# Performance work log

Measured on AMD Instinct MI355X. Metric: run time of the kernel, lower is better.

The kernel has to match this reference:

```python
import jax, jax.numpy as jnp
import numpy as np
import math

B, L, CS, CZ = 1, 512, 256, 128
H, CH, PQ, PV = 8, 32, 4, 8
NUM_BLOCKS = 8
CAT = H * CH + H * PV * 3 + H * PV + H * CZ  # 1536


def _ln(x, g, b, eps=1e-5):
    mu = jnp.mean(x, -1, keepdims=True)
    var = jnp.mean((x - mu) ** 2, -1, keepdims=True)
    return (x - mu) * jax.lax.rsqrt(var + eps) * g + b


def _quat_to_rot(bq, cq, dq):
    # BackboneUpdate: quaternion with implicit a=1, normalized (AF2 Alg. 23)
    norm = jnp.sqrt(1.0 + bq * bq + cq * cq + dq * dq)
    a = 1.0 / norm
    b = bq / norm
    c = cq / norm
    d = dq / norm
    return jnp.stack([
        jnp.stack([a * a + b * b - c * c - d * d, 2 * (b * c - a * d), 2 * (b * d + a * c)], -1),
        jnp.stack([2 * (b * c + a * d), a * a - b * b + c * c - d * d, 2 * (c * d - a * b)], -1),
        jnp.stack([2 * (b * d - a * c), 2 * (c * d + a * b), a * a - b * b - c * c + d * d], -1),
    ], -2)


def _forward(s, z, mask, ln_s_g, ln_s_b, ln_z_g, ln_z_b, w_init, b_init,
             ln_ipa_g, ln_ipa_b, ln_tr_g, ln_tr_b,
             wq, bq, wk, bk, wv, bv, wqp, bqp, wkp, bkp, wvp, bvp,
             wpb, head_w, wo, bo, wt1, bt1, wt2, bt2, wt3, bt3, wbb, bbb):
    s0 = _ln(s, ln_s_g, ln_s_b)
    zn = _ln(z, ln_z_g, ln_z_b)
    sc = s0 @ w_init + b_init
    R = jnp.broadcast_to(jnp.eye(3, dtype=s.dtype), (B, L, 3, 3))
    t = jnp.zeros((B, L, 3), s.dtype)
    wL = math.sqrt(1.0 / 3.0)
    wC = math.sqrt(2.0 / (9.0 * PQ))
    gamma = jax.nn.softplus(head_w)  # [H]
    pair_bias = jnp.einsum('bijc,ch->bhij', zn, wpb)
    mask_bias = (mask[:, None, None, :] - 1.0) * 1e9
    for i in range(NUM_BLOCKS):
        # ---- Invariant Point Attention (AF2 Alg. 22, shared weights) ----
        q = (sc @ wq + bq).reshape(B, L, H, CH)
        k = (sc @ wk + bk).reshape(B, L, H, CH)
        v = (sc @ wv + bv).reshape(B, L, H, CH)
        qp = (sc @ wqp + bqp).reshape(B, L, H, PQ, 3)
        kp = (sc @ wkp + bkp).reshape(B, L, H, PQ, 3)
        vp = (sc @ wvp + bvp).reshape(B, L, H, PV, 3)
        tb = t[:, :, None, None, :]
        qpg = jnp.einsum('blij,blhpj->blhpi', R, qp) + tb  # local -> global
        kpg = jnp.einsum('blij,blhpj->blhpi', R, kp) + tb
        vpg = jnp.einsum('blij,blhpj->blhpi', R, vp) + tb
        scal = jnp.einsum('bihc,bjhc->bhij', q, k) / math.sqrt(CH)
        # sum_p ||qpg_i - kpg_j||^2 via |q|^2 + |k|^2 - 2 q.k (avoids [B,L,L,H,P,3])
        qk = jnp.einsum('bihpx,bjhpx->bhij', qpg, kpg)
        qn = jnp.moveaxis(jnp.sum(qpg ** 2, axis=(-2, -1)), -1, 1)  # [B,H,L]
        kn = jnp.moveaxis(jnp.sum(kpg ** 2, axis=(-2, -1)), -1, 1)
        d2 = qn[..., :, None] + kn[..., None, :] - 2.0 * qk  # [B,H,L,L]
        logits = wL * (scal + pair_bias - 0.5 * wC * gamma[None, :, None, None] * d2) + mask_bias
        a = jax.nn.softmax(logits, axis=-1)
        o = jnp.einsum('bhij,bjhc->bihc', a, v).reshape(B, L, H * CH)
        optg = jnp.einsum('bhij,bjhpx->bihpx', a, vpg)
        optl = jnp.einsum('blji,blhpj->blhpi', R, optg - tb)  # R^T (o - t)
        onrm = jnp.sqrt(jnp.sum(optl ** 2, -1) + 1e-8)  # [B,L,H,PV]
        opair = jnp.einsum('bhij,bijc->bihc', a, zn).reshape(B, L, H * CZ)
        cat = jnp.concatenate([o, optl.reshape(B, L, H * PV * 3), onrm.reshape(B, L, H * PV), opair], -1)
        ipa_up = cat @ wo + bo
        sc = _ln(sc + ipa_up, ln_ipa_g, ln_ipa_b)  # dropout = identity (eval)
        # ---- transition ----
        tr = jax.nn.relu(sc @ wt1 + bt1)
        tr = jax.nn.relu(tr @ wt2 + bt2)
        tr = (tr @ wt3 + bt3) * mask[..., None]
        sc = _ln(sc + tr, ln_tr_g, ln_tr_b)
        # ---- backbone update + frame composition ----
        upd = sc @ wbb + bbb  # [B,L,6]
        dR = _quat_to_rot(upd[..., 0], upd[..., 1], upd[..., 2])
        dt = upd[..., 3:6] * mask[..., None]
        t = jnp.einsum('blij,blj->bli', R, dt) + t
        R = jnp.einsum('blij,bljk->blik', R, dR)
        if i < NUM_BLOCKS - 1:
            R = jax.lax.stop_gradient(R)  # stop_rotation_gradients
    return sc, R, t


def setup_inputs() -> dict:
    key = jax.random.key(0)
    ks = jax.random.split(key, 20)
    w = lambda k, shape, sc=0.05: jax.random.normal(k, shape, jnp.float32) * sc
    inp = dict(
        s=jax.random.normal(ks[0], (B, L, CS), jnp.float32),
        z=jax.random.normal(ks[1], (B, L, L, CZ), jnp.float32),
        mask=jnp.ones((B, L), jnp.float32),
        ln_s_g=jnp.ones((CS,), jnp.float32), ln_s_b=jnp.zeros((CS,), jnp.float32),
        ln_z_g=jnp.ones((CZ,), jnp.float32), ln_z_b=jnp.zeros((CZ,), jnp.float32),
        w_init=w(ks[2], (CS, CS)), b_init=jnp.zeros((CS,), jnp.float32),
        ln_ipa_g=jnp.ones((CS,), jnp.float32), ln_ipa_b=jnp.zeros((CS,), jnp.float32),
        ln_tr_g=jnp.ones((CS,), jnp.float32), ln_tr_b=jnp.zeros((CS,), jnp.float32),
        wq=w(ks[3], (CS, H * CH)), bq=jnp.zeros((H * CH,), jnp.float32),
        wk=w(ks[4], (CS, H * CH)), bk=jnp.zeros((H * CH,), jnp.float32),
        wv=w(ks[5], (CS, H * CH)), bv=jnp.zeros((H * CH,), jnp.float32),
        wqp=w(ks[6], (CS, H * PQ * 3)), bqp=jnp.zeros((H * PQ * 3,), jnp.float32),
        wkp=w(ks[7], (CS, H * PQ * 3)), bkp=jnp.zeros((H * PQ * 3,), jnp.float32),
        wvp=w(ks[8], (CS, H * PV * 3)), bvp=jnp.zeros((H * PV * 3,), jnp.float32),
        wpb=w(ks[9], (CZ, H)),
        head_w=jnp.zeros((H,), jnp.float32),
        wo=w(ks[10], (CAT, CS), 0.02), bo=jnp.zeros((CS,), jnp.float32),
        wt1=w(ks[11], (CS, CS)), bt1=jnp.zeros((CS,), jnp.float32),
        wt2=w(ks[12], (CS, CS)), bt2=jnp.zeros((CS,), jnp.float32),
        wt3=w(ks[13], (CS, CS)), bt3=jnp.zeros((CS,), jnp.float32),
        wbb=w(ks[14], (CS, 6)), bbb=jnp.zeros((6,), jnp.float32),
    )
    return inp


def reference(s, z, mask, ln_s_g, ln_s_b, ln_z_g, ln_z_b, w_init, b_init,
              ln_ipa_g, ln_ipa_b, ln_tr_g, ln_tr_b,
              wq, bq, wk, bk, wv, bv, wqp, bqp, wkp, bkp, wvp, bvp,
              wpb, head_w, wo, bo, wt1, bt1, wt2, bt2, wt3, bt3, wbb, bbb):
    return _forward(s, z, mask, ln_s_g, ln_s_b, ln_z_g, ln_z_b, w_init, b_init,
                    ln_ipa_g, ln_ipa_b, ln_tr_g, ln_tr_b,
                    wq, bq, wk, bk, wv, bv, wqp, bqp, wkp, bkp, wvp, bvp,
                    wpb, head_w, wo, bo, wt1, bt1, wt2, bt2, wt3, bt3, wbb, bbb)
```

## Files before the change

### kernel.cpp

```cpp
#include <hip/hip_runtime.h>
#include <hip/hip_bf16.h>
#include <hip/hip_fp16.h>
#include <math.h>

#define Lq 512
#define CSd 256
#define CZd 128
#define Hd 8
#define CHd 32
#define PQd 4
#define PVd 8
#define CATd 1536
#define NPROJ 1152

typedef __attribute__((ext_vector_type(4))) float floatx4;
typedef __attribute__((ext_vector_type(8))) short shortx8;

#define OFF_SC      0
#define OFF_PB      393216
#define OFF_P       1441792
#define OFF_QN      2031616
#define OFF_KN      2035712
#define OFF_A16     2039808
#define OFF_CAT     4136960
#define OFF_S0      4923392
#define OFF_R       5054464
#define OFF_T       5059072
#define OFF_GAMMA   5060608
#define OFF_MASKB   5060616
#define OFF_BCAT    5061128
#define OFF_WINITP  5062280
#define OFF_WT1P    5127816
#define OFF_WT2P    5193352
#define OFF_WT3P    5258888
#define OFF_WOP     5324424
#define OFF_WCATP   5717640
#define OFF_QP      6012552
#define OFF_KP      6274696
#define OFF_VP      6536840
#define OFF_ZNT     6798984

#define WLC 0.57735026918962576f
#define WCC 0.23570226039551584f
#define ISC 0.17677669529663687f

__device__ __forceinline__ float wave_sum(float v){
  #pragma unroll
  for (int m=32; m; m>>=1) v += __shfl_xor(v, m);
  return v;
}
__device__ __forceinline__ short f2bf(float v){
  __hip_bfloat16 h = (__hip_bfloat16)v;
  return __builtin_bit_cast(short, h);
}
__device__ __forceinline__ float bf2f(short s){
  unsigned u = ((unsigned)(unsigned short)s) << 16;
  return __builtin_bit_cast(float, u);
}
__device__ __forceinline__ __hip_bfloat16 s2b(short s){
  return __builtin_bit_cast(__hip_bfloat16, s);
}

__global__ __launch_bounds__(256) void k_setup(
    const float* __restrict__ bq, const float* __restrict__ bk, const float* __restrict__ bv,
    const float* __restrict__ bqp, const float* __restrict__ bkp, const float* __restrict__ bvp,
    const float* __restrict__ head_w, const float* __restrict__ mask,
    float* __restrict__ bcat, float* __restrict__ gamma,
    float* __restrict__ maskb, float* __restrict__ R, float* __restrict__ t){
  int k = blockIdx.x*256 + threadIdx.x;
  if (k < NPROJ){
    float v;
    if      (k < 256) v = bq[k];
    else if (k < 512) v = bk[k-256];
    else if (k < 768) v = bv[k-512];
    else if (k < 864) v = bqp[k-768];
    else if (k < 960) v = bkp[k-864];
    else              v = bvp[k-960];
    bcat[k] = v;
    return;
  }
  k -= NPROJ;
  if (k < Hd){ gamma[k] = log1pf(expf(head_w[k])); return; }
  k -= Hd;
  if (k < Lq){ maskb[k] = (mask[k] - 1.f)*1e9f; return; }
  k -= Lq;
  if (k < Lq){
    #pragma unroll
    for (int ii=0; ii<9; ii++) R[k*9+ii] = (ii==0||ii==4||ii==8) ? 1.f : 0.f;
    t[k*3] = 0.f; t[k*3+1] = 0.f; t[k*3+2] = 0.f;
  }
}

__global__ __launch_bounds__(256) void k_pack(
    const float* __restrict__ W, int K, int N, __hip_bfloat16* __restrict__ out){
  int idx = blockIdx.x*256 + threadIdx.x;
  if (idx >= K*N) return;
  int j = idx & 7, lane = (idx>>3) & 63, rest = idx >> 9;
  int nt = N >> 4;
  int tn = rest % nt, tk = rest / nt;
  int k = tk*32 + (lane>>4)*8 + j;
  int n = tn*16 + (lane&15);
  float v = W[(size_t)k*N + n];
  short h = f2bf(v);
  short l = f2bf(v - bf2f(h));
  size_t base = (size_t)rest*1024 + (idx & 511);
  out[base]       = s2b(h);
  out[base + 512] = s2b(l);
}

__global__ __launch_bounds__(256) void k_pack_cat(
    const float* __restrict__ wq, const float* __restrict__ wk, const float* __restrict__ wv,
    const float* __restrict__ wqp, const float* __restrict__ wkp, const float* __restrict__ wvp,
    __hip_bfloat16* __restrict__ out){
  int idx = blockIdx.x*256 + threadIdx.x;
  if (idx >= CSd*NPROJ) return;
  int j = idx & 7, lane = (idx>>3) & 63, rest = idx >> 9;
  const int nt = NPROJ >> 4;
  int tn = rest % nt, tk = rest / nt;
  int k = tk*32 + (lane>>4)*8 + j;
  int n = tn*16 + (lane&15);
  float v;
  if      (n < 256) v = wq[k*256 + n];
  else if (n < 512) v = wk[k*256 + n-256];
  else if (n < 768) v = wv[k*256 + n-512];
  else if (n < 864) v = wqp[k*96 + n-768];
  else if (n < 960) v = wkp[k*96 + n-864];
  else              v = wvp[k*192 + n-960];
  short h = f2bf(v);
  short l = f2bf(v - bf2f(h));
  size_t base = (size_t)rest*1024 + (idx & 511);
  out[base]       = s2b(h);
  out[base + 512] = s2b(l);
}

template<int NST>
__global__ __launch_bounds__(256) void k_gemm_mfma(
    const float* __restrict__ A, int K,
    const __hip_bfloat16* __restrict__ Bp, int N,
    const float* __restrict__ bias,
    float* __restrict__ Cf,
    int relu, const float* __restrict__ rowscale){
  int tid = threadIdx.x;
  int wave = tid>>6, lane = tid&63;
  int i0 = blockIdx.y*64 + wave*16;
  int n0 = blockIdx.x*(NST*16);
  int quad = lane>>4, l16 = lane&15;
  floatx4 acc[NST] = {};
  const int ntiles = N >> 4;
  const float* arow = A + (size_t)(i0 + l16)*K + quad*8;
  const __hip_bfloat16* bbase = Bp + ((size_t)(n0>>4))*1024 + (size_t)(lane&63)*8;
  for (int k0=0; k0<K; k0+=32){
    float4 v0 = *(const float4*)(arow + k0);
    float4 v1 = *(const float4*)(arow + k0 + 4);
    float av[8] = {v0.x,v0.y,v0.z,v0.w,v1.x,v1.y,v1.z,v1.w};
    shortx8 ahi, alo;
    #pragma unroll
    for (int j=0; j<8; j++){
      short h = f2bf(av[j]);
      ahi[j] = h;
      alo[j] = f2bf(av[j] - bf2f(h));
    }
    const __hip_bfloat16* bt = bbase + (size_t)(k0>>5)*ntiles*1024;
    #pragma unroll
    for (int s=0; s<NST; s++){
      shortx8 bhi = *(const shortx8*)(bt + s*1024);
      shortx8 blo = *(const shortx8*)(bt + s*1024 + 512);
      acc[s] = __builtin_amdgcn_mfma_f32_16x16x32_bf16(ahi, bhi, acc[s], 0, 0, 0);
      acc[s] = __builtin_amdgcn_mfma_f32_16x16x32_bf16(alo, bhi, acc[s], 0, 0, 0);
      acc[s] = __builtin_amdgcn_mfma_f32_16x16x32_bf16(ahi, blo, acc[s], 0, 0, 0);
    }
  }
  #pragma unroll
  for (int s=0; s<NST; s++){
    int n = n0 + s*16 + l16;
    float bs = bias ? bias[n] : 0.f;
    #pragma unroll
    for (int r=0; r<4; r++){
      int m = i0 + quad*4 + r;
      float v = acc[s][r] + bs;
      if (relu) v = fmaxf(v, 0.f);
      if (rowscale) v *= rowscale[m];
      Cf[(size_t)m*N + n] = v;
    }
  }
}

__global__ __launch_bounds__(256) void k_gemm_ipa(
    const float* __restrict__ A, const __hip_bfloat16* __restrict__ Bp,
    const float* __restrict__ bias, float* __restrict__ C0, float* __restrict__ C1){
  int tid = threadIdx.x;
  int wave = tid>>6, lane = tid&63;
  int ks = blockIdx.y >> 3;
  int i0 = (blockIdx.y & 7)*64 + wave*16;
  int n0 = blockIdx.x*16;
  int quad = lane>>4, l16 = lane&15;
  floatx4 acc = {};
  const float* arow = A + (size_t)(i0 + l16)*CATd + ks*768 + quad*8;
  const __hip_bfloat16* bbase = Bp + ((size_t)(ks*24*16 + (n0>>4)))*1024 + (size_t)lane*8;
  for (int k0=0; k0<768; k0+=32){
    float4 v0 = *(const float4*)(arow + k0);
    float4 v1 = *(const float4*)(arow + k0 + 4);
    float av[8] = {v0.x,v0.y,v0.z,v0.w,v1.x,v1.y,v1.z,v1.w};
    shortx8 ahi, alo;
    #pragma unroll
    for (int j=0; j<8; j++){
      short h = f2bf(av[j]);
      ahi[j] = h;
      alo[j] = f2bf(av[j] - bf2f(h));
    }
    const __hip_bfloat16* bt = bbase + (size_t)(k0>>5)*16*1024;
    shortx8 bhi = *(const shortx8*)bt;
    shortx8 blo = *(const shortx8*)(bt + 512);
    acc = __builtin_amdgcn_mfma_f32_16x16x32_bf16(ahi, bhi, acc, 0, 0, 0);
    acc = __builtin_amdgcn_mfma_f32_16x16x32_bf16(alo, bhi, acc, 0, 0, 0);
    acc = __builtin_amdgcn_mfma_f32_16x16x32_bf16(ahi, blo, acc, 0, 0, 0);
  }
  float* C = ks ? C1 : C0;
  int n = n0 + l16;
  float bs = ks ? 0.f : bias[n];
  #pragma unroll
  for (int r=0; r<4; r++)
    C[(size_t)(i0 + quad*4 + r)*CSd + n] = acc[r] + bs;
}

__global__ __launch_bounds__(256) void k_addln(
    const float* __restrict__ x, const float* __restrict__ y,
    const float* __restrict__ g, const float* __restrict__ b,
    float* __restrict__ out){
  __shared__ float red[4];
  int row = blockIdx.x, tid = threadIdx.x;
  float v = x[row*CSd + tid];
  if (y) v += y[row*CSd + tid];
  int wid = tid>>6, lane = tid&63;
  float s = wave_sum(v);
  if (lane==0) red[wid] = s;
  __syncthreads();
  float mu = (red[0]+red[1]+red[2]+red[3]) * (1.f/CSd);
  __syncthreads();
  float d = v - mu;
  float s2 = wave_sum(d*d);
  if (lane==0) red[wid] = s2;
  __syncthreads();
  float var = (red[0]+red[1]+red[2]+red[3]) * (1.f/CSd);
  float rs = rsqrtf(var + 1e-5f);
  out[row*CSd + tid] = d*rs*g[tid] + b[tid];
}

__global__ __launch_bounds__(1024, 4) void k_lnz_pb(
    const float* __restrict__ z, const float* __restrict__ g, const float* __restrict__ b,
    const float* __restrict__ wpb, __half* __restrict__ pb, __hip_bfloat16* __restrict__ znt){
  __shared__ float Zt[64*129];
  __shared__ float wpbl[128*12];
  __shared__ float gl[128], bl[128];
  int tid = threadIdx.x;
  size_t row0 = (size_t)blockIdx.x*64;
  int ib = (int)(row0 >> 9), j0 = (int)(row0 & 511);
  {
    int c = tid>>3, h = tid&7;
    wpbl[c*12 + h] = wpb[tid];
  }
  if (tid < 128){ gl[tid] = g[tid]; bl[tid] = b[tid]; }
  {
    int w = tid>>6, lane = tid&63;
    #pragma unroll
    for (int it=0; it<4; it++){
      int row = it*16 + w;
      const float2 v = *(const float2*)(z + (row0+row)*(size_t)CZd + lane*2);
      Zt[row*129 + lane*2]     = v.x;
      Zt[row*129 + lane*2 + 1] = v.y;
    }
  }
  __syncthreads();
  {
    int r = tid>>4, q = tid&15;
    int rot = 2*(q>>2);
    float S1=0.f, S2=0.f;
    float zv[8];
    #pragma unroll
    for (int i=0; i<8; i++){
      int ii = (i + rot) & 7;
      float v = Zt[r*129 + q*8 + ii];
      zv[i] = v;
      S1 += v; S2 += v*v;
    }
    S1 += __shfl_xor(S1,1); S2 += __shfl_xor(S2,1);
    S1 += __shfl_xor(S1,2); S2 += __shfl_xor(S2,2);
    S1 += __shfl_xor(S1,4); S2 += __shfl_xor(S2,4);
    S1 += __shfl_xor(S1,8); S2 += __shfl_xor(S2,8);
    float mu = S1 * (1.f/128.f);
    float var = S2 * (1.f/128.f) - mu*mu;
    float rs = rsqrtf(var + 1e-5f);
    float d[8] = {};
    #pragma unroll
    for (int i=0; i<8; i++){
      int ii = (i + rot) & 7;
      int c = q*8 + ii;
      float znv = (zv[i]-mu)*rs*gl[c] + bl[c];
      Zt[r*129 + c] = znv;
      const float4 w0 = *(const float4*)&wpbl[c*12];
      const float4 w1 = *(const float4*)&wpbl[c*12 + 4];
      d[0] += znv*w0.x; d[1] += znv*w0.y; d[2] += znv*w0.z; d[3] += znv*w0.w;
      d[4] += znv*w1.x; d[5] += znv*w1.y; d[6] += znv*w1.z; d[7] += znv*w1.w;
    }
    #pragma unroll
    for (int h=0; h<8; h++){
      d[h] += __shfl_xor(d[h],1);
      d[h] += __shfl_xor(d[h],2);
      d[h] += __shfl_xor(d[h],4);
      d[h] += __shfl_xor(d[h],8);
    }
    if (q == 0){
      #pragma unroll
      for (int h=0; h<8; h++)
        pb[((size_t)(h*Lq + ib))*Lq + j0 + r] = __float2half(d[h]);
    }
  }
  __syncthreads();
  {
    int jj = (tid&31)*2, cidx = tid>>5;
    unsigned short* zo = (unsigned short*)znt;
    #pragma unroll
    for (int it=0; it<4; it++){
      int c = it*32 + cidx;
      float z0 = Zt[jj*129 + c];
      float z1 = Zt[(jj+1)*129 + c];
      unsigned int o = ((unsigned int)(unsigned short)f2bf(z0)) |
                       (((unsigned int)(unsigned short)f2bf(z1)) << 16);
      *(unsigned int*)(zo + ((size_t)(ib*128 + c))*512 + j0 + jj) = o;
    }
  }
}

__global__ __launch_bounds__(256) void k_packqkv(
    const float* __restrict__ P, const float* __restrict__ R, const float* __restrict__ t,
    const float* __restrict__ gamma, int zfill,
    float* __restrict__ Qp, __hip_bfloat16* __restrict__ Kp, __hip_bfloat16* __restrict__ Vp,
    float* __restrict__ qn, float* __restrict__ kn){
  int idx = blockIdx.x*256 + threadIdx.x;
  int region = idx >> 15;
  int rem = idx & 32767;
  if (region == 0){
    int oct = rem & 7, h = (rem>>3)&7, j = rem>>6;
    float v[8] = {0.f,0.f,0.f,0.f,0.f,0.f,0.f,0.f};
    const float* Prow = P + (size_t)j*NPROJ;
    if (oct < 4){
      float4 a = *(const float4*)(Prow + 256 + h*CHd + oct*8);
      float4 b4 = *(const float4*)(Prow + 256 + h*CHd + oct*8 + 4);
      v[0]=a.x; v[1]=a.y; v[2]=a.z; v[3]=a.w; v[4]=b4.x; v[5]=b4.y; v[6]=b4.z; v[7]=b4.w;
    } else if (oct < 6){
      const float* kp = Prow + 864 + h*12;
      float4 k0 = *(const float4*)kp;
      float4 k1 = *(const float4*)(kp+4);
      float4 k2 = *(const float4*)(kp+8);
      float kv[12] = {k0.x,k0.y,k0.z,k0.w,k1.x,k1.y,k1.z,k1.w,k2.x,k2.y,k2.z,k2.w};
      float Rl[9];
      #pragma unroll
      for (int ii=0; ii<9; ii++) Rl[ii] = R[j*9+ii];
      float tv[3] = {t[j*3], t[j*3+1], t[j*3+2]};
      float gvals[12];
      #pragma unroll
      for (int p=0; p<4; p++)
        #pragma unroll
        for (int ax=0; ax<3; ax++)
          gvals[p*3+ax] = Rl[ax*3]*kv[p*3] + Rl[ax*3+1]*kv[p*3+1] + Rl[ax*3+2]*kv[p*3+2] + tv[ax];
      if (oct == 4){
        #pragma unroll
        for (int m=0; m<8; m++) v[m] = gvals[m];
      } else {
        #pragma unroll
        for (int m=0; m<4; m++) v[m] = gvals[8+m];
        float acc = 0.f;
        #pragma unroll
        for (int m=0; m<12; m++) acc += gvals[m]*gvals[m];
        kn[j*Hd + h] = acc;
      }
    } else {
      if (!zfill) return;
    }
    shortx8 hi, lo;
    #pragma unroll
    for (int m=0; m<8; m++){
      short hh = f2bf(v[m]);
      hi[m] = hh; lo[m] = f2bf(v[m] - bf2f(hh));
    }
    int kc = oct>>2, jt = j>>4, l16 = j&15, quad = oct&3;
    size_t base = (size_t)((h*2+kc)*32 + jt)*1024 + (quad*16+l16)*8;
    short* kp16 = (short*)Kp;
    *(shortx8*)(kp16 + base)       = hi;
    *(shortx8*)(kp16 + base + 512) = lo;
  } else if (region == 1){
    int n = rem & 63, h = (rem>>6)&7, jg = rem>>9;
    int jb = jg*8;
    float v[8] = {0.f,0.f,0.f,0.f,0.f,0.f,0.f,0.f};
    if (n < 32){
      #pragma unroll
      for (int m=0; m<8; m++) v[m] = P[(size_t)(jb+m)*NPROJ + 512 + h*CHd + n];
    } else if (n < 56){
      int p = (n-32)/3, ax = (n-32)%3;
      #pragma unroll
      for (int m=0; m<8; m++){
        int j = jb+m;
        const float* vp = P + (size_t)j*NPROJ + 960 + h*24 + p*3;
        const float* Rr = R + j*9 + ax*3;
        v[m] = Rr[0]*vp[0] + Rr[1]*vp[1] + Rr[2]*vp[2] + t[j*3+ax];
      }
    } else {
      if (!zfill) return;
    }
    shortx8 hi, lo;
    #pragma unroll
    for (int m=0; m<8; m++){
      short hh = f2bf(v[m]);
      hi[m] = hh; lo[m] = f2bf(v[m] - bf2f(hh));
    }
    int kc2 = jg>>2, w = n>>4, l16 = n&15, quad = jg&3;
    size_t base = (size_t)((h*16+kc2)*4 + w)*1024 + (quad*16+l16)*8;
    short* vp16 = (short*)Vp;
    *(shortx8*)(vp16 + base)       = hi;
    *(shortx8*)(vp16 + base + 512) = lo;
  } else {
    int oct = rem & 7, h = (rem>>3)&7, i = rem>>6;
    float v[8] = {0.f,0.f,0.f,0.f,0.f,0.f,0.f,0.f};
    const float* Prow = P + (size_t)i*NPROJ;
    if (oct < 4){
      float4 a = *(const float4*)(Prow + h*CHd + oct*8);
      float4 b4 = *(const float4*)(Prow + h*CHd + oct*8 + 4);
      const float sc = WLC*ISC;
      v[0]=a.x*sc; v[1]=a.y*sc; v[2]=a.z*sc; v[3]=a.w*sc;
      v[4]=b4.x*sc; v[5]=b4.y*sc; v[6]=b4.z*sc; v[7]=b4.w*sc;
    } else if (oct < 6){
      const float* qp = Prow + 768 + h*12;
      float4 k0 = *(const float4*)qp;
      float4 k1 = *(const float4*)(qp+4);
      float4 k2 = *(const float4*)(qp+8);
      float kv[12] = {k0.x,k0.y,k0.z,k0.w,k1.x,k1.y,k1.z,k1.w,k2.x,k2.y,k2.z,k2.w};
      float Rl[9];
      #pragma unroll
      for (int ii=0; ii<9; ii++) Rl[ii] = R[i*9+ii];
      float tv[3] = {t[i*3], t[i*3+1], t[i*3+2]};
      float gvals[12];
      #pragma unroll
      for (int p=0; p<4; p++)
        #pragma unroll
        for (int ax=0; ax<3; ax++)
          gvals[p*3+ax] = Rl[ax*3]*kv[p*3] + Rl[ax*3+1]*kv[p*3+1] + Rl[ax*3+2]*kv[p*3+2] + tv[ax];
      float sc = WLC*WCC*gamma[h];
      if (oct == 4){
        #pragma unroll
        for (int m=0; m<8; m++) v[m] = gvals[m]*sc;
      } else {
        #pragma unroll
        for (int m=0; m<4; m++) v[m] = gvals[8+m]*sc;
        float acc = 0.f;
        #pragma unroll
        for (int m=0; m<12; m++) acc += gvals[m]*gvals[m];
        qn[i*Hd + h] = acc;
      }
    } else {
      if (!zfill) return;
    }
    float* qrow = Qp + ((size_t)h*512 + i)*64 + oct*8;
    *(float4*)qrow       = make_float4(v[0],v[1],v[2],v[3]);
    *(float4*)(qrow + 4) = make_float4(v[4],v[5],v[6],v[7]);
  }
}

__global__ __launch_bounds__(512) void k_attn(
    const float* __restrict__ Qp, const __hip_bfloat16* __restrict__ Kp,
    const __hip_bfloat16* __restrict__ Vp,
    const float* __restrict__ qn, const float* __restrict__ kn,
    const __half* __restrict__ pb, const float* __restrict__ maskb,
    const float* __restrict__ gamma,
    const float* __restrict__ R, const float* __restrict__ t,
    __hip_bfloat16* __restrict__ a16hi,
    float* __restrict__ cat){
  __shared__ float At[8][516];
  __shared__ short AbfH[16*4*16*8];
  __shared__ short AbfL[16*4*16*8];
  __shared__ float Ot[8][36];
  __shared__ float Pv[8][68];
  __shared__ float qnL[8];
  int tid = threadIdx.x;
  int i0 = blockIdx.x*8, h = blockIdx.y;
  int wave = tid>>6, lane = tid&63, quad = lane>>4, l16 = lane&15;
  int half = wave>>2, w4 = wave&3;
  float gam = gamma[h];
  float coef = 0.5f*WLC*WCC*gam;
  if (tid < 8) qnL[tid] = qn[(i0+tid)*Hd + h];
  __syncthreads();
  const float* qrow = Qp + ((size_t)h*512 + i0 + (l16&7))*64 + quad*8;
  shortx8 qhi[2], qlo[2];
  #pragma unroll
  for (int kc=0; kc<2; kc++){
    float4 v0 = *(const float4*)(qrow + kc*32);
    float4 v1 = *(const float4*)(qrow + kc*32 + 4);
    float av[8] = {v0.x,v0.y,v0.z,v0.w,v1.x,v1.y,v1.z,v1.w};
    #pragma unroll
    for (int j=0; j<8; j++){
      short hh = f2bf(av[j]);
      qhi[kc][j] = hh; qlo[kc][j] = f2bf(av[j] - bf2f(hh));
    }
  }
  #pragma unroll
  for (int it=0; it<4; it++){
    int jt = it*8 + wave;
    floatx4 acc = {};
    #pragma unroll
    for (int kc=0; kc<2; kc++){
      const __hip_bfloat16* bt = Kp + (size_t)((h*2+kc)*32 + jt)*1024 + lane*8;
      shortx8 bhi = *(const shortx8*)bt;
      shortx8 blo = *(const shortx8*)(bt + 512);
      acc = __builtin_amdgcn_mfma_f32_16x16x32_bf16(qhi[kc], bhi, acc, 0, 0, 0);
      acc = __builtin_amdgcn_mfma_f32_16x16x32_bf16(qlo[kc], bhi, acc, 0, 0, 0);
      acc = __builtin_amdgcn_mfma_f32_16x16x32_bf16(qhi[kc], blo, acc, 0, 0, 0);
    }
    if (quad < 2){
      int j = jt*16 + l16;
      float knj = kn[j*Hd + h];
      float mbj = maskb[j];
      #pragma unroll
      for (int r=0; r<4; r++){
        int i = quad*4 + r;
        float pbv = __half2float(pb[((size_t)(h*Lq) + i0 + i)*Lq + j]);
        At[i][j] = acc[r] + WLC*pbv + mbj - coef*(qnL[i] + knj);
      }
    }
  }
  __syncthreads();
  {
    int w = wave;
    float v[8];
    float m = -1e30f;
    #pragma unroll
    for (int k=0; k<8; k++){ v[k] = At[w][lane + 64*k]; m = fmaxf(m, v[k]); }
    #pragma unroll
    for (int msk=32; msk; msk>>=1) m = fmaxf(m, __shfl_xor(m, msk));
    float ssum = 0.f;
    #pragma unroll
    for (int k=0; k<8; k++){ float e = __expf(v[k]-m); v[k]=e; ssum += e; }
    #pragma unroll
    for (int msk=32; msk; msk>>=1) ssum += __shfl_xor(ssum, msk);
    float inv = 1.f/ssum;
    #pragma unroll
    for (int k=0; k<8; k++){
      int cc = lane + 64*k;
      float p = v[k]*inv;
      short hh = f2bf(p);
      short ll = f2bf(p - bf2f(hh));
      a16hi[(((size_t)(i0+w)*16 + (cc>>5))*8 + h)*32 + (cc&31)] = s2b(hh);
      int base = ((cc>>5)*4 + ((cc>>3)&3))*16;
      int off0 = ((base + w)<<3) + (cc&7);
      int off1 = ((base + w + 8)<<3) + (cc&7);
      AbfH[off0] = hh; AbfH[off1] = hh;
      AbfL[off0] = ll; AbfL[off1] = ll;
    }
  }
  __syncthreads();
  floatx4 acc2 = {};
  #pragma unroll
  for (int kk=0; kk<8; kk++){
    int kc2 = half*8 + kk;
    int aoff = (((kc2*4 + quad)*16 + l16))<<3;
    shortx8 ahi = *(const shortx8*)&AbfH[aoff];
    shortx8 alo = *(const shortx8*)&AbfL[aoff];
    const __hip_bfloat16* bt = Vp + (size_t)((h*16+kc2)*4 + w4)*1024 + lane*8;
    shortx8 bhi = *(const shortx8*)bt;
    shortx8 blo = *(const shortx8*)(bt + 512);
    acc2 = __builtin_amdgcn_mfma_f32_16x16x32_bf16(ahi, bhi, acc2, 0, 0, 0);
    acc2 = __builtin_amdgcn_mfma_f32_16x16x32_bf16(alo, bhi, acc2, 0, 0, 0);
    acc2 = __builtin_amdgcn_mfma_f32_16x16x32_bf16(ahi, blo, acc2, 0, 0, 0);
  }
  if (half == 1 && quad < 2){
    #pragma unroll
    for (int r=0;r<4;r++) Pv[quad*4+r][w4*16+l16] = acc2[r];
  }
  __syncthreads();
  if (half == 0 && quad < 2){
    int n = w4*16 + l16;
    #pragma unroll
    for (int r=0;r<4;r++){
      int i = quad*4+r;
      float v = acc2[r] + Pv[i][n];
      if (n < 32) cat[(size_t)(i0+i)*CATd + h*CHd + n] = v;
      else        Ot[i][n-32] = v;
    }
  }
  __syncthreads();
  if (tid < 64){
    int i = tid>>3, p = tid&7, gi = i0+i;
    float o0 = Ot[i][p*3], o1 = Ot[i][p*3+1], o2 = Ot[i][p*3+2];
    float d0 = o0 - t[gi*3], d1 = o1 - t[gi*3+1], d2 = o2 - t[gi*3+2];
    const float* Rm = R + gi*9;
    float l0 = Rm[0]*d0 + Rm[3]*d1 + Rm[6]*d2;
    float l1 = Rm[1]*d0 + Rm[4]*d1 + Rm[7]*d2;
    float l2 = Rm[2]*d0 + Rm[5]*d1 + Rm[8]*d2;
    float* cr = cat + (size_t)gi*CATd;
    cr[256 + h*24 + p*3]   = l0;
    cr[256 + h*24 + p*3+1] = l1;
    cr[256 + h*24 + p*3+2] = l2;
    cr[448 + h*8 + p] = sqrtf(l0*l0 + l1*l1 + l2*l2 + 1e-8f);
  }
}

__global__ __launch_bounds__(512) void k_opair_mfma(
    const __hip_bfloat16* __restrict__ a16hi,
    const __hip_bfloat16* __restrict__ znt, float* __restrict__ cat){
  int i = blockIdx.x;
  int tid = threadIdx.x;
  int wave = tid>>6, lane = tid&63, quad = lane>>4, l16 = lane&15;
  int nt = wave;
  floatx4 acc = {};
  const __hip_bfloat16* abase_h = a16hi + ((size_t)i*16*8 + (l16&7))*32 + quad*8;
  const __hip_bfloat16* zb = znt + ((size_t)i*128 + nt*16 + l16)*512 + quad*8;
  #pragma unroll
  for (int kt=0; kt<16; kt++){
    shortx8 ah = *(const shortx8*)(abase_h + kt*256);
    shortx8 b0 = *(const shortx8*)(zb + kt*32);
    acc = __builtin_amdgcn_mfma_f32_16x16x32_bf16(ah, b0, acc, 0, 0, 0);
  }
  if (quad < 2){
    float* cr = cat + (size_t)i*CATd + 512;
    #pragma unroll
    for (int r=0; r<4; r++){
      int h = quad*4 + r;
      cr[h*CZd + nt*16 + l16] = acc[r];
    }
  }
}

__device__ __forceinline__ void gemm_bf8(
    const short* __restrict__ AHp, const short* __restrict__ ALp,
    short* __restrict__ OH, short* __restrict__ OL, float (*Yf)[260],
    const __hip_bfloat16* __restrict__ Wp, const float* __restrict__ bias,
    bool relu, int tid){
  int wave = tid>>6, lane = tid&63, quad = lane>>4, l16 = lane&15;
  floatx4 acc[2] = {};
  for (int kc=0; kc<8; kc++){
    int aoff = (((kc*4 + quad)*16 + l16))<<3;
    shortx8 ahi = *(const shortx8*)&AHp[aoff];
    shortx8 alo = *(const shortx8*)&ALp[aoff];
    #pragma unroll
    for (int ns=0; ns<2; ns++){
      const __hip_bfloat16* bt = Wp + (size_t)(kc*16 + wave*2 + ns)*1024 + lane*8;
      shortx8 bhi = *(const shortx8*)bt;
      shortx8 blo = *(const shortx8*)(bt + 512);
      acc[ns] = __builtin_amdgcn_mfma_f32_16x16x32_bf16(ahi, bhi, acc[ns], 0, 0, 0);
      acc[ns] = __builtin_amdgcn_mfma_f32_16x16x32_bf16(alo, bhi, acc[ns], 0, 0, 0);
      acc[ns] = __builtin_amdgcn_mfma_f32_16x16x32_bf16(ahi, blo, acc[ns], 0, 0, 0);
    }
  }
  #pragma unroll
  for (int ns=0; ns<2; ns++){
    int n = (wave*2+ns)*16 + l16;
    float bs = bias[n];
    #pragma unroll
    for (int r=0;r<4;r++){
      float v = acc[ns][r] + bs;
      if (relu) v = fmaxf(v, 0.f);
      int row = quad*4 + r;
      if (OH){
        short hh = f2bf(v);
        int off = ((((n>>5)*4 + ((n>>3)&3))*16 + row)<<3) + (n&7);
        OH[off] = hh;
        OL[off] = f2bf(v - bf2f(hh));
      } else {
        Yf[row][n] = v;
      }
    }
  }
}

__global__ __launch_bounds__(512) void k_mega(
    float* __restrict__ scb, const float* __restrict__ ipa, const float* __restrict__ ipa2,
    const float* __restrict__ gi_, const float* __restrict__ bi_,
    const __hip_bfloat16* __restrict__ W1, const float* __restrict__ c1,
    const __hip_bfloat16* __restrict__ W2, const float* __restrict__ c2,
    const __hip_bfloat16* __restrict__ W3, const float* __restrict__ c3,
    const float* __restrict__ gt_, const float* __restrict__ bt_,
    const float* __restrict__ mask,
    const float* __restrict__ wbb, const float* __restrict__ bbb,
    float* __restrict__ R, float* __restrict__ t){
  __shared__ float As[16][260], Bs[16][260];
  __shared__ short AH[2][4096], AL[2][4096];
  __shared__ float rA[16][33], rB[16][33];
  __shared__ float mv[16][2];
  __shared__ float u6p[16][6][2];
  int tid = threadIdx.x;
  int i0 = blockIdx.x*16;
  int r = tid>>5, c5 = tid&31, c0 = c5*8;
  float v[8];
  {
    const float* sr = scb + (size_t)(i0+r)*CSd + c0;
    const float* ir = ipa + (size_t)(i0+r)*CSd + c0;
    const float* ir2 = ipa2 + (size_t)(i0+r)*CSd + c0;
    float s1=0.f, s2=0.f;
    #pragma unroll
    for (int k2=0;k2<8;k2++){ float x = sr[k2] + ir[k2] + ir2[k2]; v[k2]=x; s1+=x; s2+=x*x; }
    rA[r][c5]=s1; rB[r][c5]=s2;
  }
  __syncthreads();
  if (tid<16){
    float s1=0.f,s2=0.f;
    #pragma unroll
    for (int c=0;c<32;c++){ s1+=rA[tid][c]; s2+=rB[tid][c]; }
    float mu = s1*(1.f/CSd), var = s2*(1.f/CSd) - mu*mu;
    mv[tid][0]=mu; mv[tid][1]=rsqrtf(var+1e-5f);
  }
  __syncthreads();
  {
    float mu=mv[r][0], rs=mv[r][1];
    #pragma unroll
    for (int k2=0;k2<8;k2++){
      int col = c0+k2;
      float o = (v[k2]-mu)*rs*gi_[col] + bi_[col];
      As[r][col] = o;
      short hh = f2bf(o);
      int off = ((((col>>5)*4 + ((col>>3)&3))*16 + r)<<3) + (col&7);
      AH[0][off] = hh;
      AL[0][off] = f2bf(o - bf2f(hh));
    }
  }
  __syncthreads();
  gemm_bf8(AH[0], AL[0], AH[1], AL[1], nullptr, W1, c1, true, tid);
  __syncthreads();
  gemm_bf8(AH[1], AL[1], AH[0], AL[0], nullptr, W2, c2, true, tid);
  __syncthreads();
  gemm_bf8(AH[0], AL[0], nullptr, nullptr, Bs, W3, c3, false, tid);
  __syncthreads();
  {
    float mk = mask[i0+r];
    float s1=0.f, s2=0.f;
    #pragma unroll
    for (int k2=0;k2<8;k2++){ float x = As[r][c0+k2] + Bs[r][c0+k2]*mk; v[k2]=x; s1+=x; s2+=x*x; }
    rA[r][c5]=s1; rB[r][c5]=s2;
  }
  __syncthreads();
  if (tid<16){
    float s1=0.f,s2=0.f;
    #pragma unroll
    for (int c=0;c<32;c++){ s1+=rA[tid][c]; s2+=rB[tid][c]; }
    float mu = s1*(1.f/CSd), var = s2*(1.f/CSd) - mu*mu;
    mv[tid][0]=mu; mv[tid][1]=rsqrtf(var+1e-5f);
  }
  __syncthreads();
  {
    float mu=mv[r][0], rs=mv[r][1];
    float* out = scb + (size_t)(i0+r)*CSd + c0;
    #pragma unroll
    for (int k2=0;k2<8;k2++){
      int col = c0+k2;
      float o = (v[k2]-mu)*rs*gt_[col] + bt_[col];
      As[r][col] = o;
      out[k2] = o;
    }
  }
  __syncthreads();
  if (tid < 192){
    int rr = tid/12, o = (tid%12)>>1, half = tid&1;
    float acc = half ? 0.f : bbb[o];
    int kb = half*128;
    for (int k2=kb; k2<kb+128; k2++) acc += As[rr][k2]*wbb[k2*6+o];
    u6p[rr][o][half] = acc;
  }
  __syncthreads();
  if (tid < 16){
    int gidx = i0 + tid;
    float uu[6];
    #pragma unroll
    for (int o=0;o<6;o++) uu[o] = u6p[tid][o][0] + u6p[tid][o][1];
    float bq = uu[0], cq = uu[1], dq = uu[2];
    float norm = sqrtf(1.f + bq*bq + cq*cq + dq*dq);
    float a = 1.f/norm, b_ = bq/norm, c_ = cq/norm, d_ = dq/norm;
    float dR[9];
    dR[0] = a*a + b_*b_ - c_*c_ - d_*d_; dR[1] = 2.f*(b_*c_ - a*d_); dR[2] = 2.f*(b_*d_ + a*c_);
    dR[3] = 2.f*(b_*c_ + a*d_); dR[4] = a*a - b_*b_ + c_*c_ - d_*d_; dR[5] = 2.f*(c_*d_ - a*b_);
    dR[6] = 2.f*(b_*d_ - a*c_); dR[7] = 2.f*(c_*d_ + a*b_); dR[8] = a*a - b_*b_ - c_*c_ + d_*d_;
    float mk = mask[gidx];
    float dt0 = uu[3]*mk, dt1 = uu[4]*mk, dt2 = uu[5]*mk;
    float Rm[9];
    #pragma unroll
    for (int ii=0; ii<9; ii++) Rm[ii] = R[gidx*9+ii];
    t[gidx*3]   += Rm[0]*dt0 + Rm[1]*dt1 + Rm[2]*dt2;
    t[gidx*3+1] += Rm[3]*dt0 + Rm[4]*dt1 + Rm[5]*dt2;
    t[gidx*3+2] += Rm[6]*dt0 + Rm[7]*dt1 + Rm[8]*dt2;
    #pragma unroll
    for (int ii=0; ii<3; ii++)
      #pragma unroll
      for (int jj=0; jj<3; jj++)
        R[gidx*9 + ii*3 + jj] = Rm[ii*3]*dR[jj] + Rm[ii*3+1]*dR[3+jj] + Rm[ii*3+2]*dR[6+jj];
  }
}

__global__ __launch_bounds__(256) void k_writeout(
    const float* __restrict__ sc, const float* __restrict__ R, const float* __restrict__ t,
    float* __restrict__ out){
  int idx = blockIdx.x*256 + threadIdx.x;
  if      (idx < 131072) out[idx] = sc[idx];
  else if (idx < 135680) out[idx] = R[idx-131072];
  else if (idx < 137216) out[idx] = t[idx-135680];
}

extern "C" void kernel_launch(void* const* d_in, const int* in_sizes, int n_in,
                              void* d_out, int out_size, void* d_ws, size_t ws_size,
                              hipStream_t stream){
  const float* s      = (const float*)d_in[0];
  const float* z      = (const float*)d_in[1];
  const float* mask   = (const float*)d_in[2];
  const float* ln_s_g = (const float*)d_in[3];
  const float* ln_s_b = (const float*)d_in[4];
  const float* ln_z_g = (const float*)d_in[5];
  const float* ln_z_b = (const float*)d_in[6];
  const float* w_init = (const float*)d_in[7];
  const float* b_init = (const float*)d_in[8];
  const float* ln_ipa_g = (const float*)d_in[9];
  const float* ln_ipa_b = (const float*)d_in[10];
  const float* ln_tr_g  = (const float*)d_in[11];
  const float* ln_tr_b  = (const float*)d_in[12];
  const float* wq = (const float*)d_in[13]; const float* bq = (const float*)d_in[14];
  const float* wk = (const float*)d_in[15]; const float* bk = (const float*)d_in[16];
  const float* wv = (const float*)d_in[17]; const float* bv = (const float*)d_in[18];
  const float* wqp = (const float*)d_in[19]; const float* bqp = (const float*)d_in[20];
  const float* wkp = (const float*)d_in[21]; const float* bkp = (const float*)d_in[22];
  const float* wvp = (const float*)d_in[23]; const float* bvp = (const float*)d_in[24];
  const float* wpb = (const float*)d_in[25];
  const float* head_w = (const float*)d_in[26];
  const float* wo = (const float*)d_in[27]; const float* bo = (const float*)d_in[28];
  const float* wt1 = (const float*)d_in[29]; const float* bt1 = (const float*)d_in[30];
  const float* wt2 = (const float*)d_in[31]; const float* bt2 = (const float*)d_in[32];
  const float* wt3 = (const float*)d_in[33]; const float* bt3 = (const float*)d_in[34];
  const float* wbb = (const float*)d_in[35]; const float* bbb = (const float*)d_in[36];

  float* W = (float*)d_ws;
  float* scb   = W + OFF_SC;
  __half*  pbb  = (__half*)(W + OFF_PB);
  float* Pb    = W + OFF_P;
  float* ipa2b = W + OFF_P + 262144;
  float* qnb   = W + OFF_QN;
  float* knb   = W + OFF_KN;
  __hip_bfloat16* a16hi = (__hip_bfloat16*)(W + OFF_A16);
  float* catb  = W + OFF_CAT;
  float* s0b   = W + OFF_S0;
  float* Rb    = W + OFF_R;
  float* tb    = W + OFF_T;
  float* gammab= W + OFF_GAMMA;
  float* maskb = W + OFF_MASKB;
  float* bcat  = W + OFF_BCAT;
  __hip_bfloat16* WinitP = (__hip_bfloat16*)(W + OFF_WINITP);
  __hip_bfloat16* Wt1P   = (__hip_bfloat16*)(W + OFF_WT1P);
  __hip_bfloat16* Wt2P   = (__hip_bfloat16*)(W + OFF_WT2P);
  __hip_bfloat16* Wt3P   = (__hip_bfloat16*)(W + OFF_WT3P);
  __hip_bfloat16* WoP    = (__hip_bfloat16*)(W + OFF_WOP);
  __hip_bfloat16* WcatP  = (__hip_bfloat16*)(W + OFF_WCATP);
  float* Qp = W + OFF_QP;
  __hip_bfloat16* Kp = (__hip_bfloat16*)(W + OFF_KP);
  __hip_bfloat16* Vp = (__hip_bfloat16*)(W + OFF_VP);
  __hip_bfloat16* znt = (__hip_bfloat16*)(W + OFF_ZNT);

  k_setup<<<9, 256, 0, stream>>>(bq,bk,bv,bqp,bkp,bvp, head_w, mask, bcat, gammab, maskb, Rb, tb);
  k_pack_cat<<<CSd*NPROJ/256, 256, 0, stream>>>(wq,wk,wv,wqp,wkp,wvp, WcatP);
  k_pack<<<256,  256, 0, stream>>>(w_init, CSd, CSd, WinitP);
  k_pack<<<1536, 256, 0, stream>>>(wo, CATd, CSd, WoP);
  k_pack<<<256,  256, 0, stream>>>(wt1, CSd, CSd, Wt1P);
  k_pack<<<256,  256, 0, stream>>>(wt2, CSd, CSd, Wt2P);
  k_pack<<<256,  256, 0, stream>>>(wt3, CSd, CSd, Wt3P);

  k_addln<<<Lq, 256, 0, stream>>>(s, nullptr, ln_s_g, ln_s_b, s0b);
  k_gemm_mfma<4><<<dim3(4,8), 256, 0, stream>>>(s0b, CSd, WinitP, CSd, b_init, scb, 0, nullptr);
  k_lnz_pb<<<Lq*Lq/64, 1024, 0, stream>>>(z, ln_z_g, ln_z_b, wpb, pbb, znt);

  for (int it=0; it<8; ++it){
    k_gemm_mfma<2><<<dim3(36,8), 256, 0, stream>>>(scb, CSd, WcatP, NPROJ, bcat, Pb, 0, nullptr);
    k_packqkv<<<384, 256, 0, stream>>>(Pb, Rb, tb, gammab, (it==0)?1:0,
                                       Qp, Kp, Vp, qnb, knb);
    k_attn<<<dim3(64,8), 512, 0, stream>>>(Qp, Kp, Vp, qnb, knb, pbb, maskb, gammab, Rb, tb,
                                           a16hi, catb);
    k_opair_mfma<<<Lq, 512, 0, stream>>>(a16hi, znt, catb);
    k_gemm_ipa<<<dim3(16,16), 256, 0, stream>>>(catb, WoP, bo, Pb, ipa2b);
    k_mega<<<32, 512, 0, stream>>>(scb, Pb, ipa2b, ln_ipa_g, ln_ipa_b,
                                   Wt1P, bt1, Wt2P, bt2, Wt3P, bt3,
                                   ln_tr_g, ln_tr_b, mask, wbb, bbb, Rb, tb);
  }
  k_writeout<<<536, 256, 0, stream>>>(scb, Rb, tb, (float*)d_out);
}
```

Before: 887.6 us.

## Pre-split projection inputs to bf16, widen attention tiles, retune LN-z stores

```diff
diff --git a/kernel.cpp b/kernel.cpp
--- a/kernel.cpp
+++ b/kernel.cpp
@@ -38,7 +38,8 @@
 #define OFF_QP      6012552
 #define OFF_KP      6274696
 #define OFF_VP      6536840
-#define OFF_ZNT     6798984
+#define OFF_SCA16   6798984
+#define OFF_ZNT     6930056
 
 #define WLC 0.57735026918962576f
 #define WCC 0.23570226039551584f
@@ -185,6 +186,62 @@
   }
 }
 
+__global__ __launch_bounds__(256) void k_cvtA(
+    const float* __restrict__ sc, short* __restrict__ scA16){
+  int idx = blockIdx.x*256 + threadIdx.x;
+  int i = idx>>5, c5 = idx&31;
+  int c0 = c5*8, kc = c5>>2, quad = c5&3;
+  float4 v0 = *(const float4*)(sc + (size_t)i*CSd + c0);
+  float4 v1 = *(const float4*)(sc + (size_t)i*CSd + c0 + 4);
+  float av[8] = {v0.x,v0.y,v0.z,v0.w,v1.x,v1.y,v1.z,v1.w};
+  shortx8 hi, lo;
+  #pragma unroll
+  for (int j=0; j<8; j++){
+    short h = f2bf(av[j]);
+    hi[j] = h; lo[j] = f2bf(av[j] - bf2f(h));
+  }
+  size_t off = ((size_t)(kc*512 + i)*4 + quad)*8;
+  *(shortx8*)(scA16 + off)          = hi;
+  *(shortx8*)(scA16 + off + 131072) = lo;
+}
+
+__global__ __launch_bounds__(256) void k_gemm_proj(
+    const short* __restrict__ scA16,
+    const __hip_bfloat16* __restrict__ Bp,
+    const float* __restrict__ bias,
+    float* __restrict__ Cf){
+  int tid = threadIdx.x;
+  int wave = tid>>6, lane = tid&63;
+  int i0 = blockIdx.y*64 + wave*16;
+  int n0 = blockIdx.x*32;
+  int quad = lane>>4, l16 = lane&15;
+  floatx4 acc[2] = {};
+  const short* abase = scA16 + ((size_t)(i0 + l16)*4 + quad)*8;
+  const __hip_bfloat16* bbase = Bp + ((size_t)(n0>>4))*1024 + (size_t)lane*8;
+  #pragma unroll
+  for (int kc=0; kc<8; kc++){
+    shortx8 ahi = *(const shortx8*)(abase + kc*16384);
+    shortx8 alo = *(const shortx8*)(abase + kc*16384 + 131072);
+    const __hip_bfloat16* bt = bbase + (size_t)kc*72*1024;
+    #pragma unroll
+    for (int s=0; s<2; s++){
+      shortx8 bhi = *(const shortx8*)(bt + s*1024);
+      shortx8 blo = *(const shortx8*)(bt + s*1024 + 512);
+      acc[s] = __builtin_amdgcn_mfma_f32_16x16x32_bf16(ahi, bhi, acc[s], 0, 0, 0);
+      acc[s] = __builtin_amdgcn_mfma_f32_16x16x32_bf16(alo, bhi, acc[s], 0, 0, 0);
+      acc[s] = __builtin_amdgcn_mfma_f32_16x16x32_bf16(ahi, blo, acc[s], 0, 0, 0);
+    }
+  }
+  #pragma unroll
+  for (int s=0; s<2; s++){
+    int n = n0 + s*16 + l16;
+    float bs = bias[n];
+    #pragma unroll
+    for (int r=0; r<4; r++)
+      Cf[(size_t)(i0 + quad*4 + r)*NPROJ + n] = acc[s][r] + bs;
+  }
+}
+
 __global__ __launch_bounds__(256) void k_gemm_ipa(
     const float* __restrict__ A, const __hip_bfloat16* __restrict__ Bp,
     const float* __restrict__ bias, float* __restrict__ C0, float* __restrict__ C1){
@@ -250,14 +307,14 @@
     const float* __restrict__ z, const float* __restrict__ g, const float* __restrict__ b,
     const float* __restrict__ wpb, __half* __restrict__ pb, __hip_bfloat16* __restrict__ znt){
   __shared__ float Zt[64*129];
-  __shared__ float wpbl[128*12];
+  __shared__ float wpbht[8*129];
   __shared__ float gl[128], bl[128];
   int tid = threadIdx.x;
   size_t row0 = (size_t)blockIdx.x*64;
   int ib = (int)(row0 >> 9), j0 = (int)(row0 & 511);
   {
     int c = tid>>3, h = tid&7;
-    wpbl[c*12 + h] = wpb[tid];
+    wpbht[h*129 + c] = wpb[tid];
   }
   if (tid < 128){ gl[tid] = g[tid]; bl[tid] = b[tid]; }
   {
@@ -297,10 +354,8 @@
       int c = q*8 + ii;
       float znv = (zv[i]-mu)*rs*gl[c] + bl[c];
       Zt[r*129 + c] = znv;
-      const float4 w0 = *(const float4*)&wpbl[c*12];
-      const float4 w1 = *(const float4*)&wpbl[c*12 + 4];
-      d[0] += znv*w0.x; d[1] += znv*w0.y; d[2] += znv*w0.z; d[3] += znv*w0.w;
-      d[4] += znv*w1.x; d[5] += znv*w1.y; d[6] += znv*w1.z; d[7] += znv*w1.w;
+      #pragma unroll
+      for (int h=0; h<8; h++) d[h] += znv * wpbht[h*129 + c];
     }
     #pragma unroll
     for (int h=0; h<8; h++){
@@ -317,17 +372,19 @@
   }
   __syncthreads();
   {
-    int jj = (tid&31)*2, cidx = tid>>5;
+    int c = tid>>3, jg = tid&7;
+    int jb = jg*8;
+    unsigned int o[4];
+    #pragma unroll
+    for (int k=0; k<4; k++){
+      float z0 = Zt[(jb+2*k)*129 + c];
+      float z1 = Zt[(jb+2*k+1)*129 + c];
+      o[k] = ((unsigned int)(unsigned short)f2bf(z0)) |
+             (((unsigned int)(unsigned short)f2bf(z1)) << 16);
+    }
     unsigned short* zo = (unsigned short*)znt;
-    #pragma unroll
-    for (int it=0; it<4; it++){
-      int c = it*32 + cidx;
-      float z0 = Zt[jj*129 + c];
-      float z1 = Zt[(jj+1)*129 + c];
-      unsigned int o = ((unsigned int)(unsigned short)f2bf(z0)) |
-                       (((unsigned int)(unsigned short)f2bf(z1)) << 16);
-      *(unsigned int*)(zo + ((size_t)(ib*128 + c))*512 + j0 + jj) = o;
-    }
+    uint4 pk = make_uint4(o[0],o[1],o[2],o[3]);
+    *(uint4*)(zo + ((size_t)(ib*128 + c))*512 + j0 + jb) = pk;
   }
 }
 
@@ -465,7 +522,7 @@
   }
 }
 
-__global__ __launch_bounds__(512) void k_attn(
+__global__ __launch_bounds__(1024) void k_attn(
     const float* __restrict__ Qp, const __hip_bfloat16* __restrict__ Kp,
     const __hip_bfloat16* __restrict__ Vp,
     const float* __restrict__ qn, const float* __restrict__ kn,
@@ -474,21 +531,21 @@
     const float* __restrict__ R, const float* __restrict__ t,
     __hip_bfloat16* __restrict__ a16hi,
     float* __restrict__ cat){
-  __shared__ float At[8][516];
+  __shared__ float At[16][516];
   __shared__ short AbfH[16*4*16*8];
   __shared__ short AbfL[16*4*16*8];
-  __shared__ float Ot[8][36];
-  __shared__ float Pv[8][68];
-  __shared__ float qnL[8];
+  __shared__ float Pv[3][16][68];
+  __shared__ float Ot[16][36];
+  __shared__ float qnL[16];
   int tid = threadIdx.x;
-  int i0 = blockIdx.x*8, h = blockIdx.y;
+  int i0 = blockIdx.x*16, h = blockIdx.y;
   int wave = tid>>6, lane = tid&63, quad = lane>>4, l16 = lane&15;
-  int half = wave>>2, w4 = wave&3;
+  int kg = wave>>2, ng = wave&3;
   float gam = gamma[h];
   float coef = 0.5f*WLC*WCC*gam;
-  if (tid < 8) qnL[tid] = qn[(i0+tid)*Hd + h];
-  __syncthreads();
-  const float* qrow = Qp + ((size_t)h*512 + i0 + (l16&7))*64 + quad*8;
+  if (tid < 16) qnL[tid] = qn[(i0+tid)*Hd + h];
+  __syncthreads();
+  const float* qrow = Qp + ((size_t)h*512 + i0 + l16)*64 + quad*8;
   shortx8 qhi[2], qlo[2];
   #pragma unroll
   for (int kc=0; kc<2; kc++){
@@ -502,8 +559,8 @@
     }
   }
   #pragma unroll
-  for (int it=0; it<4; it++){
-    int jt = it*8 + wave;
+  for (int it=0; it<2; it++){
+    int jt = it*16 + wave;
     floatx4 acc = {};
     #pragma unroll
     for (int kc=0; kc<2; kc++){
@@ -514,16 +571,14 @@
       acc = __builtin_amdgcn_mfma_f32_16x16x32_bf16(qlo[kc], bhi, acc, 0, 0, 0);
       acc = __builtin_amdgcn_mfma_f32_16x16x32_bf16(qhi[kc], blo, acc, 0, 0, 0);
     }
-    if (quad < 2){
-      int j = jt*16 + l16;
-      float knj = kn[j*Hd + h];
-      float mbj = maskb[j];
-      #pragma unroll
-      for (int r=0; r<4; r++){
-        int i = quad*4 + r;
-        float pbv = __half2float(pb[((size_t)(h*Lq) + i0 + i)*Lq + j]);
-        At[i][j] = acc[r] + WLC*pbv + mbj - coef*(qnL[i] + knj);
-      }
+    int j = jt*16 + l16;
+    float knj = kn[j*Hd + h];
+    float mbj = maskb[j];
+    #pragma unroll
+    for (int r=0; r<4; r++){
+      int i = quad*4 + r;
+      float pbv = __half2float(pb[((size_t)(h*Lq) + i0 + i)*Lq + j]);
+      At[i][j] = acc[r] + WLC*pbv + mbj - coef*(qnL[i] + knj);
     }
   }
   __syncthreads();
@@ -548,45 +603,43 @@
       short hh = f2bf(p);
       short ll = f2bf(p - bf2f(hh));
       a16hi[(((size_t)(i0+w)*16 + (cc>>5))*8 + h)*32 + (cc&31)] = s2b(hh);
-      int base = ((cc>>5)*4 + ((cc>>3)&3))*16;
-      int off0 = ((base + w)<<3) + (cc&7);
-      int off1 = ((base + w + 8)<<3) + (cc&7);
-      AbfH[off0] = hh; AbfH[off1] = hh;
-      AbfL[off0] = ll; AbfL[off1] = ll;
+      int off = ((((cc>>5)*4 + ((cc>>3)&3))*16 + w)<<3) + (cc&7);
+      AbfH[off] = hh;
+      AbfL[off] = ll;
     }
   }
   __syncthreads();
   floatx4 acc2 = {};
   #pragma unroll
-  for (int kk=0; kk<8; kk++){
-    int kc2 = half*8 + kk;
+  for (int kk=0; kk<4; kk++){
+    int kc2 = kg*4 + kk;
     int aoff = (((kc2*4 + quad)*16 + l16))<<3;
     shortx8 ahi = *(const shortx8*)&AbfH[aoff];
     shortx8 alo = *(const shortx8*)&AbfL[aoff];
-    const __hip_bfloat16* bt = Vp + (size_t)((h*16+kc2)*4 + w4)*1024 + lane*8;
+    const __hip_bfloat16* bt = Vp + (size_t)((h*16+kc2)*4 + ng)*1024 + lane*8;
     shortx8 bhi = *(const shortx8*)bt;
     shortx8 blo = *(const shortx8*)(bt + 512);
     acc2 = __builtin_amdgcn_mfma_f32_16x16x32_bf16(ahi, bhi, acc2, 0, 0, 0);
     acc2 = __builtin_amdgcn_mfma_f32_16x16x32_bf16(alo, bhi, acc2, 0, 0, 0);
     acc2 = __builtin_amdgcn_mfma_f32_16x16x32_bf16(ahi, blo, acc2, 0, 0, 0);
   }
-  if (half == 1 && quad < 2){
-    #pragma unroll
-    for (int r=0;r<4;r++) Pv[quad*4+r][w4*16+l16] = acc2[r];
-  }
-  __syncthreads();
-  if (half == 0 && quad < 2){
-    int n = w4*16 + l16;
+  if (kg > 0){
+    #pragma unroll
+    for (int r=0;r<4;r++) Pv[kg-1][quad*4+r][ng*16+l16] = acc2[r];
+  }
+  __syncthreads();
+  if (kg == 0){
+    int n = ng*16 + l16;
     #pragma unroll
     for (int r=0;r<4;r++){
       int i = quad*4+r;
-      float v = acc2[r] + Pv[i][n];
+      float v = acc2[r] + Pv[0][i][n] + Pv[1][i][n] + Pv[2][i][n];
       if (n < 32) cat[(size_t)(i0+i)*CATd + h*CHd + n] = v;
       else        Ot[i][n-32] = v;
     }
   }
   __syncthreads();
-  if (tid < 64){
+  if (tid < 128){
     int i = tid>>3, p = tid&7, gi = i0+i;
     float o0 = Ot[i][p*3], o1 = Ot[i][p*3+1], o2 = Ot[i][p*3+2];
     float d0 = o0 - t[gi*3], d1 = o1 - t[gi*3+1], d2 = o2 - t[gi*3+2];
@@ -679,7 +732,7 @@
     const float* __restrict__ gt_, const float* __restrict__ bt_,
     const float* __restrict__ mask,
     const float* __restrict__ wbb, const float* __restrict__ bbb,
-    float* __restrict__ R, float* __restrict__ t){
+    float* __restrict__ R, float* __restrict__ t, short* __restrict__ scA16){
   __shared__ float As[16][260], Bs[16][260];
   __shared__ short AH[2][4096], AL[2][4096];
   __shared__ float rA[16][33], rB[16][33];
@@ -746,13 +799,19 @@
   {
     float mu=mv[r][0], rs=mv[r][1];
     float* out = scb + (size_t)(i0+r)*CSd + c0;
+    shortx8 hi, lo;
     #pragma unroll
     for (int k2=0;k2<8;k2++){
       int col = c0+k2;
       float o = (v[k2]-mu)*rs*gt_[col] + bt_[col];
       As[r][col] = o;
       out[k2] = o;
-    }
+      short hh = f2bf(o);
+      hi[k2] = hh; lo[k2] = f2bf(o - bf2f(hh));
+    }
+    size_t off = ((size_t)((c5>>2)*512 + i0 + r)*4 + (c5&3))*8;
+    *(shortx8*)(scA16 + off)          = hi;
+    *(shortx8*)(scA16 + off + 131072) = lo;
   }
   __syncthreads();
   if (tid < 192){
@@ -854,6 +913,7 @@
   float* Qp = W + OFF_QP;
   __hip_bfloat16* Kp = (__hip_bfloat16*)(W + OFF_KP);
   __hip_bfloat16* Vp = (__hip_bfloat16*)(W + OFF_VP);
+  short* scA16 = (short*)(W + OFF_SCA16);
   __hip_bfloat16* znt = (__hip_bfloat16*)(W + OFF_ZNT);
 
   k_setup<<<9, 256, 0, stream>>>(bq,bk,bv,bqp,bkp,bvp, head_w, mask, bcat, gammab, maskb, Rb, tb);
@@ -866,19 +926,20 @@
 
   k_addln<<<Lq, 256, 0, stream>>>(s, nullptr, ln_s_g, ln_s_b, s0b);
   k_gemm_mfma<4><<<dim3(4,8), 256, 0, stream>>>(s0b, CSd, WinitP, CSd, b_init, scb, 0, nullptr);
+  k_cvtA<<<64, 256, 0, stream>>>(scb, scA16);
   k_lnz_pb<<<Lq*Lq/64, 1024, 0, stream>>>(z, ln_z_g, ln_z_b, wpb, pbb, znt);
 
   for (int it=0; it<8; ++it){
-    k_gemm_mfma<2><<<dim3(36,8), 256, 0, stream>>>(scb, CSd, WcatP, NPROJ, bcat, Pb, 0, nullptr);
+    k_gemm_proj<<<dim3(36,8), 256, 0, stream>>>(scA16, WcatP, bcat, Pb);
     k_packqkv<<<384, 256, 0, stream>>>(Pb, Rb, tb, gammab, (it==0)?1:0,
                                        Qp, Kp, Vp, qnb, knb);
-    k_attn<<<dim3(64,8), 512, 0, stream>>>(Qp, Kp, Vp, qnb, knb, pbb, maskb, gammab, Rb, tb,
-                                           a16hi, catb);
+    k_attn<<<dim3(32,8), 1024, 0, stream>>>(Qp, Kp, Vp, qnb, knb, pbb, maskb, gammab, Rb, tb,
+                                            a16hi, catb);
     k_opair_mfma<<<Lq, 512, 0, stream>>>(a16hi, znt, catb);
     k_gemm_ipa<<<dim3(16,16), 256, 0, stream>>>(catb, WoP, bo, Pb, ipa2b);
     k_mega<<<32, 512, 0, stream>>>(scb, Pb, ipa2b, ln_ipa_g, ln_ipa_b,
                                    Wt1P, bt1, Wt2P, bt2, Wt3P, bt3,
-                                   ln_tr_g, ln_tr_b, mask, wbb, bbb, Rb, tb);
+                                   ln_tr_g, ln_tr_b, mask, wbb, bbb, Rb, tb, scA16);
   }
   k_writeout<<<536, 256, 0, stream>>>(scb, Rb, tb, (float*)d_out);
 }
```

New measurement: 845.2 us. -4.8%, faster.
